# Performance work log

Measured on AMD Instinct MI355X. Metric: run time of the kernel, lower is better.

Reference implementation:

```python
import math
import jax, jax.numpy as jnp
import numpy as np

N_TOKENS = 2048
HIDDEN = 2880
HEAD_DIM = 64
N_HEADS = 64
N_KV = 8
Q_MULT = N_HEADS // N_KV  # 8
SLIDING_WINDOW = 128      # layer_idx=0 -> even -> window active
RMS_EPS = 1e-5
SM_SCALE = 1.0 / math.sqrt(HEAD_DIM)
ROPE_THETA = 150000.0
INIT_CTX = 4096
SCALING_FACTOR = 32.0
NTK_ALPHA = 1.0
NTK_BETA = 32.0
QKV_DIM = HEAD_DIM * (N_HEADS + 2 * N_KV)  # 5120


def _rope_cos_sin(n_tokens):
    # YaRN/NTK-scaled inverse frequencies (scaling_factor > 1 branch)
    freq = ROPE_THETA ** (jnp.arange(0, HEAD_DIM, 2, dtype=jnp.float32) / HEAD_DIM)
    concentration = 0.1 * math.log(SCALING_FACTOR) + 1.0
    d_half = HEAD_DIM / 2
    low = d_half * math.log(INIT_CTX / (NTK_BETA * 2 * math.pi)) / math.log(ROPE_THETA)
    high = d_half * math.log(INIT_CTX / (NTK_ALPHA * 2 * math.pi)) / math.log(ROPE_THETA)
    interpolation = 1.0 / (SCALING_FACTOR * freq)
    extrapolation = 1.0 / freq
    ramp = (jnp.arange(d_half, dtype=jnp.float32) - low) / (high - low)
    mask = 1.0 - jnp.clip(ramp, 0.0, 1.0)
    inv_freq = interpolation * (1.0 - mask) + extrapolation * mask
    pos = jnp.arange(n_tokens, dtype=jnp.float32)
    freqs = pos[:, None] * inv_freq[None, :]        # [n, d/2]
    return jnp.cos(freqs) * concentration, jnp.sin(freqs) * concentration


def _apply_rotary(x, cos, sin):
    # x: [n, h, d]; cos/sin: [n, d/2]
    c = cos[:, None, :]
    s = sin[:, None, :]
    x1, x2 = jnp.split(x, 2, axis=-1)
    return jnp.concatenate([x1 * c - x2 * s, x2 * c + x1 * s], axis=-1)


def setup_inputs() -> dict:
    key = jax.random.key(0)
    ks = jax.random.split(key, 4)
    x = jax.random.normal(ks[0], (N_TOKENS, HIDDEN), dtype=jnp.float32)
    norm_scale = jnp.ones((HIDDEN,), dtype=jnp.float32)
    sinks = jax.random.normal(ks[1], (N_HEADS,), dtype=jnp.float32)
    w_qkv = jax.random.normal(ks[2], (QKV_DIM, HIDDEN), dtype=jnp.float32) * 0.02
    b_qkv = jnp.zeros((QKV_DIM,), dtype=jnp.float32)
    w_out = jax.random.normal(ks[3], (HIDDEN, N_HEADS * HEAD_DIM), dtype=jnp.float32) * 0.02
    b_out = jnp.zeros((HIDDEN,), dtype=jnp.float32)
    return {"x": x, "norm_scale": norm_scale, "sinks": sinks,
            "w_qkv": w_qkv, "b_qkv": b_qkv, "w_out": w_out, "b_out": b_out}


def reference(x, norm_scale, sinks, w_qkv, b_qkv, w_out, b_out):
    n = x.shape[0]
    # RMSNorm (fp32 math as in original)
    t = x.astype(jnp.float32)
    t = t * jax.lax.rsqrt(jnp.mean(t * t, axis=-1, keepdims=True) + RMS_EPS)
    t = (t * norm_scale).astype(x.dtype)
    # QKV projection (torch Linear: y = x @ W^T + b)
    qkv = t @ w_qkv.T + b_qkv
    q = qkv[:, : N_HEADS * HEAD_DIM].reshape(n, N_KV, Q_MULT, HEAD_DIM)
    k = qkv[:, N_HEADS * HEAD_DIM:(N_HEADS + N_KV) * HEAD_DIM].reshape(n, N_KV, HEAD_DIM)
    v = qkv[:, (N_HEADS + N_KV) * HEAD_DIM:].reshape(n, N_KV, HEAD_DIM)
    # RoPE
    cos, sin = _rope_cos_sin(n)
    q = _apply_rotary(q.reshape(n, N_HEADS, HEAD_DIM), cos, sin).reshape(n, N_KV, Q_MULT, HEAD_DIM)
    k = _apply_rotary(k, cos, sin)
    # GQA attention scores: [kv_heads, q_mult, q, k]
    qk = jnp.einsum('qhmd,khd->hmqk', q, k) * SM_SCALE
    # causal + sliding-window mask: allow j <= i and j > i - SLIDING_WINDOW
    i = jnp.arange(n)[:, None]
    j = jnp.arange(n)[None, :]
    allowed = (j <= i) & (j > i - SLIDING_WINDOW)
    neg_inf = jnp.asarray(-jnp.inf, dtype=qk.dtype)
    qk = jnp.where(allowed[None, None, :, :], qk, neg_inf)
    # append learned sink logit per head, softmax, then drop sink column
    sink_logits = jnp.broadcast_to(
        sinks.reshape(N_KV, Q_MULT, 1, 1), (N_KV, Q_MULT, n, 1)).astype(qk.dtype)
    logits = jnp.concatenate([qk, sink_logits], axis=-1)
    weights = jax.nn.softmax(logits, axis=-1)[..., :-1]
    attn = jnp.einsum('hmqk,khd->qhmd', weights, v).reshape(n, N_HEADS * HEAD_DIM)
    return x + attn @ w_out.T + b_out
```

## Files before the change

kernel.cpp:

```cpp
#include <hip/hip_runtime.h>
#include <hip/hip_bf16.h>
#include <math.h>

typedef __attribute__((ext_vector_type(8))) short short8;
typedef __attribute__((ext_vector_type(4))) float f32x4;

#define NTOK 2048
#define HID  2880
#define QKVD 5120
#define KOFF 4096
#define VOFF 4608
#define ATTD 4096

__device__ __forceinline__ unsigned short f2bf(float f) {
  union { float f; unsigned int u; } v; v.f = f;
  unsigned int u = v.u;
  unsigned int r = (u + 0x7FFFu + ((u >> 16) & 1u)) >> 16;
  return (unsigned short)r;
}
__device__ __forceinline__ float bf2f(unsigned short h) {
  union { unsigned int u; float f; } v; v.u = ((unsigned int)h) << 16; return v.f;
}
__device__ __forceinline__ void gload_lds16(const unsigned short* g, unsigned short* l) {
  __builtin_amdgcn_global_load_lds(
      (const __attribute__((address_space(1))) unsigned int*)g,
      (__attribute__((address_space(3))) unsigned int*)l, 16, 0, 0);
}
#define MFMA16(a, b, c) __builtin_amdgcn_mfma_f32_16x16x32_bf16((a), (b), (c), 0, 0, 0)

__global__ __launch_bounds__(256) void prep_kernel(
    const float* __restrict__ x, const float* __restrict__ scale,
    unsigned short* __restrict__ t,
    const float* __restrict__ w1, unsigned short* __restrict__ w1bf,
    const float* __restrict__ w2, unsigned short* __restrict__ w2bf,
    float* __restrict__ ctab, float* __restrict__ stab) {
  __shared__ float red[4];
  const int bid = blockIdx.x;
  const int tid = threadIdx.x;
  if (bid < 2048) {
    const float4* xr = (const float4*)(x + (size_t)bid * HID);
    const float4* sc = (const float4*)scale;
    float ss = 0.f;
    for (int c = tid; c < HID / 4; c += 256) {
      float4 v = xr[c];
      ss += v.x * v.x + v.y * v.y + v.z * v.z + v.w * v.w;
    }
    #pragma unroll
    for (int m = 1; m < 64; m <<= 1) ss += __shfl_xor(ss, m);
    if ((tid & 63) == 0) red[tid >> 6] = ss;
    __syncthreads();
    float tot = red[0] + red[1] + red[2] + red[3];
    float rs = rsqrtf(tot / (float)HID + 1e-5f);
    for (int c = tid; c < HID / 4; c += 256) {
      float4 v = xr[c];
      float4 s4 = sc[c];
      ushort4 o;
      o.x = f2bf(v.x * rs * s4.x); o.y = f2bf(v.y * rs * s4.y);
      o.z = f2bf(v.z * rs * s4.z); o.w = f2bf(v.w * rs * s4.w);
      *(ushort4*)&t[(size_t)bid * HID + c * 4] = o;
    }
  } else if (bid < 8528) {
    const float* src; unsigned short* dst; long base0;
    if (bid < 5648) { src = w1; dst = w1bf; base0 = (long)(bid - 2048) * 1024; }
    else            { src = w2; dst = w2bf; base0 = (long)(bid - 5648) * 1024; }
    #pragma unroll
    for (int k2 = 0; k2 < 4; ++k2) {
      long base = (base0 + k2 * 256 + tid) * 4;
      float4 v = *(const float4*)&src[base];
      ushort4 o;
      o.x = f2bf(v.x); o.y = f2bf(v.y); o.z = f2bf(v.z); o.w = f2bf(v.w);
      *(ushort4*)&dst[base] = o;
    }
  } else {
    int idx = (bid - 8528) * 256 + tid;
    int pos = idx >> 5, i = idx & 31;
    const double theta = 150000.0;
    const double two_pi = 6.283185307179586476925286766559;
    double freq = pow(theta, (double)i / 32.0);
    double interp = 1.0 / (32.0 * freq);
    double extrap = 1.0 / freq;
    double low  = 32.0 * log(4096.0 / (32.0 * two_pi)) / log(theta);
    double high = 32.0 * log(4096.0 / (1.0  * two_pi)) / log(theta);
    double ramp = ((double)i - low) / (high - low);
    ramp = ramp < 0.0 ? 0.0 : (ramp > 1.0 ? 1.0 : ramp);
    double maskv = 1.0 - ramp;
    double inv = interp * (1.0 - maskv) + extrap * maskv;
    double ang = (double)pos * inv;
    double conc = 0.1 * log(32.0) + 1.0;
    ctab[idx] = (float)(cos(ang) * conc);
    stab[idx] = (float)(sin(ang) * conc);
  }
}

template<int BN, bool RESID>
__global__ __launch_bounds__(256, 2) void gemm_kernel(
    const unsigned short* __restrict__ A, const unsigned short* __restrict__ B,
    const float* __restrict__ bias, const float* __restrict__ resid,
    void* __restrict__ Cout, int K, int NC) {
  constexpr int NF = BN / 32;
  __shared__ unsigned short sA[2][8192];
  __shared__ unsigned short sB[2][BN * 64];

  const int tid = threadIdx.x;
  const int q8 = gridDim.x >> 3;
  const int sw = ((int)blockIdx.x & 7) * q8 + ((int)blockIdx.x >> 3);
  const int m0 = (sw & 15) * 128;
  const int n0 = (sw >> 4) * BN;

  const int lane = tid & 63, wid = tid >> 6;
  const int fr = lane & 15, fq = lane >> 4;
  const int wr = wid >> 1, wc = wid & 1;
  const int swz = (fr & 7) << 4;
  const int r_st = tid >> 3;
  const int c8_st = ((tid & 7) ^ ((tid >> 3) & 7)) * 8;
  const int wlds = wid << 9;

  const unsigned short* Ag = A + (size_t)(m0 + r_st) * K + c8_st;
  const unsigned short* Bg = B + (size_t)(n0 + r_st) * K + c8_st;

  f32x4 acc[4][NF] = {};
  const int NT = K >> 6;

  auto LDA_ = [&](int bs, int mf, int ks) -> short8 {
    int row = wr * 64 + mf * 16 + fr;
    int cb = (ks * 64 + fq * 16) ^ swz;
    return *(const short8*)((const char*)&sA[bs][0] + row * 128 + cb);
  };
  auto LDB_ = [&](int bs, int nf, int ks) -> short8 {
    int row = wc * (NF * 16) + nf * 16 + fr;
    int cb = (ks * 64 + fq * 16) ^ swz;
    return *(const short8*)((const char*)&sB[bs][0] + row * 128 + cb);
  };
  auto issue_tile = [&](int tt, int b) {
    const unsigned short* Agt = Ag + (size_t)tt * 64;
    const unsigned short* Bgt = Bg + (size_t)tt * 64;
    #pragma unroll
    for (int s = 0; s < 4; ++s)
      gload_lds16(Agt + (size_t)(s * 32) * K, &sA[b][s * 2048 + wlds]);
    #pragma unroll
    for (int s = 0; s < NF; ++s)
      gload_lds16(Bgt + (size_t)(s * 32) * K, &sB[b][s * 2048 + wlds]);
  };

  issue_tile(0, 0);

  for (int t = 0; t < NT; ++t) {
    const int cu = t & 1;
    asm volatile("s_waitcnt vmcnt(0)" ::: "memory");
    __builtin_amdgcn_s_barrier();
    __builtin_amdgcn_sched_barrier(0);
    if (t + 1 < NT) issue_tile(t + 1, cu ^ 1);
    short8 afr0[4], bfr0[NF], afr1[4], bfr1[NF];
    #pragma unroll
    for (int mf = 0; mf < 4; ++mf) afr0[mf] = LDA_(cu, mf, 0);
    #pragma unroll
    for (int nf = 0; nf < NF; ++nf) bfr0[nf] = LDB_(cu, nf, 0);
    #pragma unroll
    for (int mf = 0; mf < 4; ++mf) afr1[mf] = LDA_(cu, mf, 1);
    #pragma unroll
    for (int nf = 0; nf < NF; ++nf) bfr1[nf] = LDB_(cu, nf, 1);
    __builtin_amdgcn_s_setprio(1);
    #pragma unroll
    for (int mf = 0; mf < 4; ++mf)
      #pragma unroll
      for (int nf = 0; nf < NF; ++nf)
        acc[mf][nf] = MFMA16(afr0[mf], bfr0[nf], acc[mf][nf]);
    #pragma unroll
    for (int mf = 0; mf < 4; ++mf)
      #pragma unroll
      for (int nf = 0; nf < NF; ++nf)
        acc[mf][nf] = MFMA16(afr1[mf], bfr1[nf], acc[mf][nf]);
    __builtin_amdgcn_s_setprio(0);
  }

  if (!RESID) {
    unsigned short* C = (unsigned short*)Cout;
    #pragma unroll
    for (int mf = 0; mf < 4; ++mf)
      #pragma unroll
      for (int nf = 0; nf < NF; ++nf)
        #pragma unroll
        for (int r = 0; r < 4; ++r) {
          int row = m0 + wr * 64 + mf * 16 + fq * 4 + r;
          int col = n0 + wc * (NF * 16) + nf * 16 + fr;
          C[(size_t)row * NC + col] = f2bf(acc[mf][nf][r] + bias[col]);
        }
  } else {
    float* C = (float*)Cout;
    #pragma unroll
    for (int mf = 0; mf < 4; ++mf)
      #pragma unroll
      for (int nf = 0; nf < NF; ++nf)
        #pragma unroll
        for (int r = 0; r < 4; ++r) {
          int row = m0 + wr * 64 + mf * 16 + fq * 4 + r;
          int col = n0 + wc * (NF * 16) + nf * 16 + fr;
          C[(size_t)row * NC + col] = acc[mf][nf][r] + bias[col] + resid[(size_t)row * NC + col];
        }
  }
}

__global__ __launch_bounds__(512) void attn_kernel(
    const unsigned short* __restrict__ qkv, const float* __restrict__ sinks,
    const float* __restrict__ ctab, const float* __restrict__ stab,
    unsigned short* __restrict__ attn) {
  const int tile = blockIdx.x;
  const int h = blockIdx.y;
  const int q0 = tile * 64;
  const int kbase = q0 - 127;

  __shared__ unsigned short Qsh[64][72];
  __shared__ unsigned short Ksh[192][72];
  __shared__ unsigned short Vt[64][200];
  __shared__ unsigned short Wsh[64][200];
  __shared__ float rowpart[4][64];
  __shared__ float invsum[64];

  const int tid = threadIdx.x;

  #pragma unroll
  for (int it = 0; it < 2; ++it) {
    int lin = tid + it * 512;
    if (lin < 768) {
      int r = lin >> 2, cp = lin & 3;
      int j = kbase + r;
      short8 oa = {}, ob = {};
      if (j >= 0 && j < NTOK) {
        const unsigned short* kp = &qkv[(size_t)j * QKVD + KOFF + h * 64 + cp * 8];
        short8 xa = *(const short8*)kp;
        short8 xb = *(const short8*)(kp + 32);
        #pragma unroll
        for (int e = 0; e < 8; ++e) {
          float c = ctab[j * 32 + cp * 8 + e], s = stab[j * 32 + cp * 8 + e];
          float x1 = bf2f((unsigned short)xa[e]), x2 = bf2f((unsigned short)xb[e]);
          oa[e] = (short)f2bf(x1 * c - x2 * s);
          ob[e] = (short)f2bf(x2 * c + x1 * s);
        }
      }
      *(short8*)&Ksh[r][cp * 8] = oa;
      *(short8*)&Ksh[r][cp * 8 + 32] = ob;
    }
  }
  {
    const int d = tid & 63;
    const int jg0 = tid >> 6;
    const unsigned short* vcol = qkv + VOFF + (size_t)h * 64 + d;
    #pragma unroll
    for (int it = 0; it < 3; ++it) {
      int jg = jg0 + it * 8;
      int jb = kbase + jg * 8;
      unsigned int e01 = 0, e23 = 0, e45 = 0, e67 = 0;
      if (jb >= 0) {
        e01 = (unsigned int)vcol[(size_t)(jb + 0) * QKVD]
            | ((unsigned int)vcol[(size_t)(jb + 1) * QKVD] << 16);
        e23 = (unsigned int)vcol[(size_t)(jb + 2) * QKVD]
            | ((unsigned int)vcol[(size_t)(jb + 3) * QKVD] << 16);
        e45 = (unsigned int)vcol[(size_t)(jb + 4) * QKVD]
            | ((unsigned int)vcol[(size_t)(jb + 5) * QKVD] << 16);
        e67 = (unsigned int)vcol[(size_t)(jb + 6) * QKVD]
            | ((unsigned int)vcol[(size_t)(jb + 7) * QKVD] << 16);
      } else if (jb + 7 >= 0) {
        unsigned short ev[8];
        #pragma unroll
        for (int e = 0; e < 8; ++e)
          ev[e] = (jb + e >= 0) ? vcol[(size_t)(jb + e) * QKVD] : (unsigned short)0;
        e01 = ev[0] | ((unsigned int)ev[1] << 16);
        e23 = ev[2] | ((unsigned int)ev[3] << 16);
        e45 = ev[4] | ((unsigned int)ev[5] << 16);
        e67 = ev[6] | ((unsigned int)ev[7] << 16);
      }
      *(uint4*)&Vt[d][jg * 8] = make_uint4(e01, e23, e45, e67);
    }
  }

  const int lane = tid & 63;
  const int wid = tid >> 6;
  const int fr = lane & 15;
  const int fq = lane >> 4;
  const int fc = fq * 8;
  const int rg = wid >> 2;
  const int cg = wid & 3;
  const int wk0 = cg * 48;

  for (int qm = 0; qm < 8; ++qm) {
    const int gh = h * 8 + qm;
    if (tid < 256) {
      int r = tid >> 2, cp = tid & 3;
      int i = q0 + r;
      const unsigned short* qp = &qkv[(size_t)i * QKVD + gh * 64 + cp * 8];
      short8 xa = *(const short8*)qp;
      short8 xb = *(const short8*)(qp + 32);
      short8 oa, ob;
      #pragma unroll
      for (int e = 0; e < 8; ++e) {
        float c = ctab[i * 32 + cp * 8 + e], s = stab[i * 32 + cp * 8 + e];
        float x1 = bf2f((unsigned short)xa[e]), x2 = bf2f((unsigned short)xb[e]);
        oa[e] = (short)f2bf(x1 * c - x2 * s);
        ob[e] = (short)f2bf(x2 * c + x1 * s);
      }
      *(short8*)&Qsh[r][cp * 8] = oa;
      *(short8*)&Qsh[r][cp * 8 + 32] = ob;
    }
    __syncthreads();

    f32x4 sc[2][3] = {};
    #pragma unroll
    for (int k0 = 0; k0 < 64; k0 += 32) {
      short8 qa[2], kb[3];
      #pragma unroll
      for (int mi = 0; mi < 2; ++mi)
        qa[mi] = *(const short8*)&Qsh[rg * 32 + mi * 16 + fr][k0 + fc];
      #pragma unroll
      for (int ni = 0; ni < 3; ++ni)
        kb[ni] = *(const short8*)&Ksh[wk0 + ni * 16 + fr][k0 + fc];
      #pragma unroll
      for (int mi = 0; mi < 2; ++mi)
        #pragma unroll
        for (int ni = 0; ni < 3; ++ni)
          sc[mi][ni] = MFMA16(qa[mi], kb[ni], sc[mi][ni]);
    }

    #pragma unroll
    for (int mi = 0; mi < 2; ++mi)
      #pragma unroll
      for (int r = 0; r < 4; ++r) {
        int row = rg * 32 + mi * 16 + fq * 4 + r;
        int i = q0 + row;
        float rs = 0.f;
        #pragma unroll
        for (int ni = 0; ni < 3; ++ni) {
          int kk = wk0 + ni * 16 + fr;
          int j = kbase + kk;
          bool valid = (j >= 0) && (j <= i) && (j > i - 128);
          float pw = valid ? __expf(sc[mi][ni][r] * 0.125f) : 0.f;
          sc[mi][ni][r] = pw;
          rs += pw;
        }
        rs += __shfl_xor(rs, 1);
        rs += __shfl_xor(rs, 2);
        rs += __shfl_xor(rs, 4);
        rs += __shfl_xor(rs, 8);
        #pragma unroll
        for (int ni = 0; ni < 3; ++ni)
          Wsh[row][wk0 + ni * 16 + fr] = f2bf(sc[mi][ni][r]);
        if (fr == 0) rowpart[cg][row] = rs;
      }
    __syncthreads();

    if (tid < 64) {
      float tot = rowpart[0][tid] + rowpart[1][tid] + rowpart[2][tid] + rowpart[3][tid];
      invsum[tid] = 1.f / (tot + __expf(sinks[gh]));
    }

    f32x4 pv[2] = {};
    #pragma unroll
    for (int k0 = 0; k0 < 192; k0 += 32) {
      short8 pa[2];
      #pragma unroll
      for (int mi = 0; mi < 2; ++mi)
        pa[mi] = *(const short8*)&Wsh[rg * 32 + mi * 16 + fr][k0 + fc];
      short8 vb = *(const short8*)&Vt[cg * 16 + fr][k0 + fc];
      #pragma unroll
      for (int mi = 0; mi < 2; ++mi)
        pv[mi] = MFMA16(pa[mi], vb, pv[mi]);
    }
    __syncthreads();

    #pragma unroll
    for (int mi = 0; mi < 2; ++mi)
      #pragma unroll
      for (int r = 0; r < 4; ++r) {
        int row = rg * 32 + mi * 16 + fq * 4 + r;
        float inv = invsum[row];
        int col = cg * 16 + fr;
        attn[(size_t)(q0 + row) * ATTD + gh * 64 + col] = f2bf(pv[mi][r] * inv);
      }
  }
}

extern "C" void kernel_launch(void* const* d_in, const int* in_sizes, int n_in,
                              void* d_out, int out_size, void* d_ws, size_t ws_size,
                              hipStream_t stream) {
  const float* x          = (const float*)d_in[0];
  const float* norm_scale = (const float*)d_in[1];
  const float* sinks      = (const float*)d_in[2];
  const float* w_qkv      = (const float*)d_in[3];
  const float* b_qkv      = (const float*)d_in[4];
  const float* w_out      = (const float*)d_in[5];
  const float* b_out      = (const float*)d_in[6];
  float* out = (float*)d_out;

  char* ws = (char*)d_ws;
  unsigned short* qkv_bf = (unsigned short*)(ws);
  unsigned short* t_bf   = (unsigned short*)(ws + 20971520);
  unsigned short* attn_b = (unsigned short*)(ws + 20971520);
  unsigned short* w1bf   = (unsigned short*)(ws + 20971520 + 16777216);
  unsigned short* w2bf   = (unsigned short*)(ws + 20971520 + 16777216 + 29491200);
  float* ctab = (float*)(ws + 20971520 + 16777216 + 29491200 + 23592960);
  float* stab = ctab + NTOK * 32;

  prep_kernel<<<dim3(8784), dim3(256), 0, stream>>>(
      x, norm_scale, t_bf, w_qkv, w1bf, w_out, w2bf, ctab, stab);
  gemm_kernel<160, false><<<dim3(512), dim3(256), 0, stream>>>(
      t_bf, w1bf, b_qkv, nullptr, (void*)qkv_bf, HID, QKVD);
  attn_kernel<<<dim3(32, 8), dim3(512), 0, stream>>>(qkv_bf, sinks, ctab, stab, attn_b);
  gemm_kernel<96, true><<<dim3(480), dim3(256), 0, stream>>>(
      attn_b, w2bf, b_out, x, (void*)out, ATTD, HID);
}
```

Before: 188.6 us.

## Single-buffer GEMM LDS tiles to raise occupancy via more blocks per CU

Removes the double-buffered LDS prefetch in the GEMM kernel: each iteration now barriers, loads the current tile, waits, and barriers again before computing. This halves the shared memory per block and raises the launch-bounds minimum blocks per CU (4 for the QKV GEMM, 5 for the output GEMM). The aim is to hide memory latency through occupancy rather than software pipelining. In exchange, loads no longer overlap compute within a block, and the tighter register budget may cause spills.

```diff
diff --git a/kernel.cpp b/kernel.cpp
--- a/kernel.cpp
+++ b/kernel.cpp
@@ -92,14 +92,14 @@
   }
 }
 
-template<int BN, bool RESID>
-__global__ __launch_bounds__(256, 2) void gemm_kernel(
+template<int BN, bool RESID, int MINB>
+__global__ __launch_bounds__(256, MINB) void gemm_kernel(
     const unsigned short* __restrict__ A, const unsigned short* __restrict__ B,
     const float* __restrict__ bias, const float* __restrict__ resid,
     void* __restrict__ Cout, int K, int NC) {
   constexpr int NF = BN / 32;
-  __shared__ unsigned short sA[2][8192];
-  __shared__ unsigned short sB[2][BN * 64];
+  __shared__ unsigned short sA[8192];
+  __shared__ unsigned short sB[BN * 64];
 
   const int tid = threadIdx.x;
   const int q8 = gridDim.x >> 3;
@@ -121,44 +121,42 @@
   f32x4 acc[4][NF] = {};
   const int NT = K >> 6;
 
-  auto LDA_ = [&](int bs, int mf, int ks) -> short8 {
+  auto LDA_ = [&](int mf, int ks) -> short8 {
     int row = wr * 64 + mf * 16 + fr;
     int cb = (ks * 64 + fq * 16) ^ swz;
-    return *(const short8*)((const char*)&sA[bs][0] + row * 128 + cb);
+    return *(const short8*)((const char*)&sA[0] + row * 128 + cb);
   };
-  auto LDB_ = [&](int bs, int nf, int ks) -> short8 {
+  auto LDB_ = [&](int nf, int ks) -> short8 {
     int row = wc * (NF * 16) + nf * 16 + fr;
     int cb = (ks * 64 + fq * 16) ^ swz;
-    return *(const short8*)((const char*)&sB[bs][0] + row * 128 + cb);
+    return *(const short8*)((const char*)&sB[0] + row * 128 + cb);
   };
-  auto issue_tile = [&](int tt, int b) {
+  auto issue_tile = [&](int tt) {
     const unsigned short* Agt = Ag + (size_t)tt * 64;
     const unsigned short* Bgt = Bg + (size_t)tt * 64;
     #pragma unroll
     for (int s = 0; s < 4; ++s)
-      gload_lds16(Agt + (size_t)(s * 32) * K, &sA[b][s * 2048 + wlds]);
+      gload_lds16(Agt + (size_t)(s * 32) * K, &sA[s * 2048 + wlds]);
     #pragma unroll
     for (int s = 0; s < NF; ++s)
-      gload_lds16(Bgt + (size_t)(s * 32) * K, &sB[b][s * 2048 + wlds]);
+      gload_lds16(Bgt + (size_t)(s * 32) * K, &sB[s * 2048 + wlds]);
   };
 
-  issue_tile(0, 0);
-
   for (int t = 0; t < NT; ++t) {
-    const int cu = t & 1;
+    asm volatile("s_barrier" ::: "memory");
+    issue_tile(t);
     asm volatile("s_waitcnt vmcnt(0)" ::: "memory");
-    __builtin_amdgcn_s_barrier();
+    asm volatile("s_barrier" ::: "memory");
     __builtin_amdgcn_sched_barrier(0);
-    if (t + 1 < NT) issue_tile(t + 1, cu ^ 1);
     short8 afr0[4], bfr0[NF], afr1[4], bfr1[NF];
     #pragma unroll
-    for (int mf = 0; mf < 4; ++mf) afr0[mf] = LDA_(cu, mf, 0);
-    #pragma unroll
-    for (int nf = 0; nf < NF; ++nf) bfr0[nf] = LDB_(cu, nf, 0);
-    #pragma unroll
-    for (int mf = 0; mf < 4; ++mf) afr1[mf] = LDA_(cu, mf, 1);
-    #pragma unroll
-    for (int nf = 0; nf < NF; ++nf) bfr1[nf] = LDB_(cu, nf, 1);
+    for (int mf = 0; mf < 4; ++mf) afr0[mf] = LDA_(mf, 0);
+    #pragma unroll
+    for (int nf = 0; nf < NF; ++nf) bfr0[nf] = LDB_(nf, 0);
+    #pragma unroll
+    for (int mf = 0; mf < 4; ++mf) afr1[mf] = LDA_(mf, 1);
+    #pragma unroll
+    for (int nf = 0; nf < NF; ++nf) bfr1[nf] = LDB_(nf, 1);
     __builtin_amdgcn_s_setprio(1);
     #pragma unroll
     for (int mf = 0; mf < 4; ++mf)
@@ -401,9 +399,9 @@
 
   prep_kernel<<<dim3(8784), dim3(256), 0, stream>>>(
       x, norm_scale, t_bf, w_qkv, w1bf, w_out, w2bf, ctab, stab);
-  gemm_kernel<160, false><<<dim3(512), dim3(256), 0, stream>>>(
+  gemm_kernel<160, false, 4><<<dim3(512), dim3(256), 0, stream>>>(
       t_bf, w1bf, b_qkv, nullptr, (void*)qkv_bf, HID, QKVD);
   attn_kernel<<<dim3(32, 8), dim3(512), 0, stream>>>(qkv_bf, sinks, ctab, stab, attn_b);
-  gemm_kernel<96, true><<<dim3(480), dim3(256), 0, stream>>>(
+  gemm_kernel<96, true, 5><<<dim3(480), dim3(256), 0, stream>>>(
       attn_b, w2bf, b_out, x, (void*)out, ATTD, HID);
 }
```

New measurement: 672.2 us. 3.56x slower.
